# Performance work log

Measured on AMD Instinct MI355X. Metric: run time of the kernel, lower is better.

Reference implementation:

```python
import jax, jax.numpy as jnp
import numpy as np

DIM_IN = 1024
DIM_OUT = 1024


def setup_inputs() -> dict:
    key = jax.random.key(0)
    k1, k2, k3, k4 = jax.random.split(key, 4)
    X = jax.random.normal(k1, (4, 2048, DIM_IN), dtype=jnp.float32)
    s = 1.0 / np.sqrt(DIM_IN)
    Wq = jax.random.normal(k2, (DIM_IN, DIM_OUT), dtype=jnp.float32) * s
    Wk = jax.random.normal(k3, (DIM_IN, DIM_OUT), dtype=jnp.float32) * s
    Wv = jax.random.normal(k4, (DIM_IN, DIM_OUT), dtype=jnp.float32) * s
    return {"X": X, "Wq": Wq, "Wk": Wk, "Wv": Wv}


def reference(X, Wq, Wk, Wv):
    # X: [B, T, Din]; projections (qkv_bias=False)
    q = jnp.einsum('btd,de->bte', X, Wq)   # [B, T, Dout]
    k = jnp.einsum('btd,de->bte', X, Wk)
    v = jnp.einsum('btd,de->bte', X, Wv)
    T = X.shape[1]
    scores = jnp.einsum('bqe,bke->bqk', q, k)  # [B, T, T]
    causal = jnp.tril(jnp.ones((T, T), dtype=bool))  # mask upper triangle (future)
    scores = jnp.where(causal, scores, -jnp.inf)
    # scale=True: divide by sqrt(d); -inf stays -inf so order vs mask is irrelevant
    scores = scores / jnp.sqrt(jnp.asarray(k.shape[-1], dtype=scores.dtype))
    weights = jax.nn.softmax(scores, axis=-1)
    # dropout p=0.0 -> identity
    return jnp.einsum('bqk,bke->bqe', weights, v)
```

## Files before the change

kernel.cpp:

```cpp
#include <hip/hip_runtime.h>
#include <hip/hip_bf16.h>

typedef unsigned short u16;
typedef __bf16 bf16x8 __attribute__((ext_vector_type(8)));
typedef float f32x4 __attribute__((ext_vector_type(4)));
typedef unsigned short u16x8 __attribute__((ext_vector_type(8)));
typedef unsigned short u16x4 __attribute__((ext_vector_type(4)));

__device__ __forceinline__ float bf2f(u16 u) {
  unsigned int x = ((unsigned int)u) << 16;
  return __builtin_bit_cast(float, x);
}
__device__ __forceinline__ u16 f2bf(float f) {
  unsigned int x = __builtin_bit_cast(unsigned int, f);
  x = x + 0x7FFFu + ((x >> 16) & 1u);
  return (u16)(x >> 16);
}

__device__ __forceinline__ void gload_lds16(const u16* g, u16* l) {
  __builtin_amdgcn_global_load_lds(
      (const __attribute__((address_space(1))) unsigned int*)(unsigned long long)(uintptr_t)g,
      (__attribute__((address_space(3))) unsigned int*)(unsigned int)(uintptr_t)l,
      16, 0, 0);
}

__global__ __launch_bounds__(256) void prep_kernel(const float* __restrict__ X,
                                                   const float* __restrict__ Wq,
                                                   const float* __restrict__ Wk,
                                                   const float* __restrict__ Wv,
                                                   u16* __restrict__ Xb,
                                                   u16* __restrict__ Wqr,
                                                   u16* __restrict__ Wkr,
                                                   u16* __restrict__ WG) {
  const int id = blockIdx.x;
  const int tid = threadIdx.x;
  if (id < 5120) {
    const float* src;
    u16* dst;
    float scale = 1.0f;
    long i;
    if (id < 4096) {
      src = X; dst = Xb; i = ((long)id * 256 + tid) * 8;
    } else if (id < 4608) {
      src = Wq; dst = Wqr; scale = 1.0f / 32.0f;
      i = ((long)(id - 4096) * 256 + tid) * 8;
    } else {
      src = Wk; dst = Wkr;
      i = ((long)(id - 4608) * 256 + tid) * 8;
    }
    float4 a = *reinterpret_cast<const float4*>(src + i);
    float4 b = *reinterpret_cast<const float4*>(src + i + 4);
    u16x8 o;
    o[0] = f2bf(a.x * scale); o[1] = f2bf(a.y * scale);
    o[2] = f2bf(a.z * scale); o[3] = f2bf(a.w * scale);
    o[4] = f2bf(b.x * scale); o[5] = f2bf(b.y * scale);
    o[6] = f2bf(b.z * scale); o[7] = f2bf(b.w * scale);
    *reinterpret_cast<u16x8*>(dst + i) = o;
    return;
  }
  __shared__ u16 t[64][72];
  const int id2 = id - 5120;
  u16* out = WG + 1048576;
  const int c0 = (id2 & 15) * 64;
  const int r0 = (id2 >> 4) * 64;
#pragma unroll
  for (int i = 0; i < 4; ++i) {
    int slot = tid + 256 * i;
    int lr = slot >> 4;
    int lc4 = slot & 15;
    float4 v = *reinterpret_cast<const float4*>(Wv + (long)(r0 + lr) * 1024 + c0 + lc4 * 4);
    t[lr][lc4 * 4 + 0] = f2bf(v.x);
    t[lr][lc4 * 4 + 1] = f2bf(v.y);
    t[lr][lc4 * 4 + 2] = f2bf(v.z);
    t[lr][lc4 * 4 + 3] = f2bf(v.w);
  }
  __syncthreads();
#pragma unroll
  for (int i = 0; i < 2; ++i) {
    int slot = tid + 256 * i;
    int orow = slot >> 3;
    int oc = slot & 7;
    u16x8 o;
#pragma unroll
    for (int j = 0; j < 8; ++j) o[j] = t[oc * 8 + j][orow];
    *reinterpret_cast<u16x8*>(out + (long)(c0 + orow) * 1024 + r0 + oc * 8) = o;
  }
}

template <int MODE>
__global__ __launch_bounds__(256, 2) void gemm128(const u16* __restrict__ A,
                                                  const u16* __restrict__ B,
                                                  u16* __restrict__ C,
                                                  u16* __restrict__ Vt) {
  int bm, bn;
  if constexpr (MODE == 0) {
    bm = blockIdx.x >> 3;
    bn = blockIdx.x & 7;
  } else {
    const int id = blockIdx.x;
    const int xcd = id & 7, j = id >> 3;
    bn = (xcd & 1) * 8 + (j & 7);
    bm = ((xcd >> 1) << 4) + (j >> 3);
  }
  const int m0 = bm * 128, n0 = bn * 128;
  const int K = 1024;

  bool vblk = false;
  if constexpr (MODE == 1) vblk = (bn >> 3) == 1;

  __shared__ u16 ldsA[2][8192];
  __shared__ u16 ldsB[2][8192];

  const int tid = threadIdx.x;
  const int lane = tid & 63;
  const int wid = tid >> 6;
  const int wm = wid >> 1, wn = wid & 1;
  const int l16 = lane & 15, lh = lane >> 4;
  const int srow = lane >> 3;
  const int scol = ((lane & 7) ^ srow) * 8;
  const int rsw = l16 & 7;

  f32x4 acc[4][4];
#pragma unroll
  for (int mi = 0; mi < 4; ++mi)
#pragma unroll
    for (int ni = 0; ni < 4; ++ni) acc[mi][ni] = (f32x4)(0.0f);

  auto stage = [&](int d, int k0) {
#pragma unroll
    for (int s = 0; s < 4; ++s) {
      const int seg = wid * 4 + s;
      const int row = seg * 8 + srow;
      gload_lds16(A + (long)(m0 + row) * K + k0 + scol, &ldsA[d][seg * 512]);
      gload_lds16(B + (long)(n0 + row) * K + k0 + scol, &ldsB[d][seg * 512]);
    }
  };

  stage(0, 0);
  int cur = 0;
  for (int k0 = 0; k0 < K; k0 += 64) {
    __syncthreads();
    if (k0 + 64 < K) stage(cur ^ 1, k0 + 64);
#pragma unroll
    for (int kk = 0; kk < 2; ++kk) {
      bf16x8 af[4], bfr[4];
#pragma unroll
      for (int mi = 0; mi < 4; ++mi)
        af[mi] = *reinterpret_cast<const bf16x8*>(
            &ldsA[cur][(wm * 64 + mi * 16 + l16) * 64 + (((kk * 4 + lh) ^ rsw)) * 8]);
#pragma unroll
      for (int ni = 0; ni < 4; ++ni)
        bfr[ni] = *reinterpret_cast<const bf16x8*>(
            &ldsB[cur][(wn * 64 + ni * 16 + l16) * 64 + (((kk * 4 + lh) ^ rsw)) * 8]);
      if (!vblk) {
#pragma unroll
        for (int mi = 0; mi < 4; ++mi)
#pragma unroll
          for (int ni = 0; ni < 4; ++ni)
            acc[mi][ni] = __builtin_amdgcn_mfma_f32_16x16x32_bf16(bfr[ni], af[mi], acc[mi][ni], 0, 0, 0);
      } else {
#pragma unroll
        for (int mi = 0; mi < 4; ++mi)
#pragma unroll
          for (int ni = 0; ni < 4; ++ni)
            acc[mi][ni] = __builtin_amdgcn_mfma_f32_16x16x32_bf16(af[mi], bfr[ni], acc[mi][ni], 0, 0, 0);
      }
    }
    cur ^= 1;
  }

  if (!vblk) {
    const int col0 = (MODE == 0) ? n0 : (bn & 7) * 128;
    const long rown = (long)(m0 + wm * 64 + l16);
    const int coln = col0 + wn * 64 + lh * 4;
#pragma unroll
    for (int mi = 0; mi < 4; ++mi)
#pragma unroll
      for (int ni = 0; ni < 4; ++ni) {
        u16x4 o;
#pragma unroll
        for (int r = 0; r < 4; ++r) o[r] = f2bf(acc[mi][ni][r]);
        *reinterpret_cast<u16x4*>(&C[(rown + mi * 16) * 1024 + coln + ni * 16]) = o;
      }
  } else {
    const int b = m0 >> 11;
    const int t0 = (m0 & 2047) + wm * 64 + lh * 4;
    const int e0 = (bn & 7) * 128 + wn * 64 + l16;
#pragma unroll
    for (int mi = 0; mi < 4; ++mi)
#pragma unroll
      for (int ni = 0; ni < 4; ++ni) {
        u16x4 o;
#pragma unroll
        for (int r = 0; r < 4; ++r) o[r] = f2bf(acc[mi][ni][r]);
        *reinterpret_cast<u16x4*>(
            &Vt[(long)b * 2097152 + (long)(e0 + ni * 16) * 2048 + t0 + mi * 16]) = o;
      }
  }
}

__global__ __launch_bounds__(256, 3) void gemm_s(const u16* __restrict__ T1,
                                                 const u16* __restrict__ Xb,
                                                 u16* __restrict__ Sg,
                                                 float* __restrict__ Sums) {
  const int id = blockIdx.x;
  const int x = id & 7;
  const int q = id >> 3;
  const int bz = q / 34;
  int u = q - bz * 34;
  int qr, kc;
  const int n1 = 32 - 2 * x;
  if (u < n1) { kc = x;      qr = 2 * x + u; }
  else        { kc = 15 - x; qr = 30 - 2 * x + (u - n1); }
  const int m0 = qr * 64, n0 = kc * 128;
  const int K = 1024;

  const u16* A = T1 + (long)bz * 2097152;
  const u16* B = Xb + (long)bz * 2097152;

  __shared__ u16 ldsA[2][4096];
  __shared__ u16 ldsB[2][8192];

  const int tid = threadIdx.x;
  const int lane = tid & 63;
  const int wn = tid >> 6;
  const int l16 = lane & 15, lh = lane >> 4;
  const int strow = tid >> 3;
  const int scol = ((tid & 7) ^ (strow & 7)) * 8;
  const int rsw = l16 & 7;

  f32x4 acc[4][2];
#pragma unroll
  for (int mi = 0; mi < 4; ++mi)
#pragma unroll
    for (int ni = 0; ni < 2; ++ni) acc[mi][ni] = (f32x4)(0.0f);

  auto stage = [&](int d, int k0) {
#pragma unroll
    for (int l = 0; l < 2; ++l)
      gload_lds16(A + (long)(m0 + l * 32 + strow) * K + k0 + scol,
                  &ldsA[d][l * 2048 + tid * 8]);
#pragma unroll
    for (int l = 0; l < 4; ++l)
      gload_lds16(B + (long)(n0 + l * 32 + strow) * K + k0 + scol,
                  &ldsB[d][l * 2048 + tid * 8]);
  };

  stage(0, 0);
  int cur = 0;
  for (int k0 = 0; k0 < K; k0 += 64) {
    __syncthreads();
    if (k0 + 64 < K) stage(cur ^ 1, k0 + 64);
#pragma unroll
    for (int kk = 0; kk < 2; ++kk) {
      bf16x8 af[4], bfr[2];
#pragma unroll
      for (int mi = 0; mi < 4; ++mi)
        af[mi] = *reinterpret_cast<const bf16x8*>(
            &ldsA[cur][(mi * 16 + l16) * 64 + (((kk * 4 + lh) ^ rsw)) * 8]);
#pragma unroll
      for (int ni = 0; ni < 2; ++ni)
        bfr[ni] = *reinterpret_cast<const bf16x8*>(
            &ldsB[cur][(wn * 32 + ni * 16 + l16) * 64 + (((kk * 4 + lh) ^ rsw)) * 8]);
#pragma unroll
      for (int mi = 0; mi < 4; ++mi)
#pragma unroll
        for (int ni = 0; ni < 2; ++ni)
          acc[mi][ni] = __builtin_amdgcn_mfma_f32_16x16x32_bf16(bfr[ni], af[mi], acc[mi][ni], 0, 0, 0);
    }
    cur ^= 1;
  }

  u16* C = Sg + (long)bz * 4194304;
  float* sums = Sums + (long)bz * 2048;
  const int coln = n0 + wn * 32 + lh * 4;
#pragma unroll
  for (int mi = 0; mi < 4; ++mi) {
    const int gr = m0 + mi * 16 + l16;
    float rs = 0.0f;
#pragma unroll
    for (int ni = 0; ni < 2; ++ni) {
      u16x4 o;
#pragma unroll
      for (int r = 0; r < 4; ++r) {
        const int gc = coln + ni * 16 + r;
        const float e = (gc <= gr) ? __expf(acc[mi][ni][r]) : 0.0f;
        const u16 ub = f2bf(e);
        o[r] = ub;
        rs += bf2f(ub);
      }
      *reinterpret_cast<u16x4*>(&C[(long)gr * 2048 + coln + ni * 16]) = o;
    }
    rs += __shfl_xor(rs, 16);
    rs += __shfl_xor(rs, 32);
    if (lh == 0) atomicAdd(&sums[gr], rs);
  }
}

__global__ __launch_bounds__(512, 2) void gemm_pv(const u16* __restrict__ Ag,
                                                  const u16* __restrict__ Bg,
                                                  float* __restrict__ Cg,
                                                  const float* __restrict__ Sums) {
  const int id = blockIdx.x;
  const int x = id & 7;
  const int q = id >> 3;
  const int f = (q ^ (q >> 5)) & 1;
  const int i5 = ((q >> 1) & 15) | (((q >> 5) & 1) << 4);
  const int bmb = i5 & 7;
  const int bz = (i5 >> 3) & 3;
  const int bm = f ? (15 - bmb) : bmb;
  const int bn = x;
  const int K = 2048;

  const u16* A = Ag + (long)bz * 4194304;
  const u16* B = Bg + (long)bz * 2097152;
  const int m0 = bm * 128, n0 = bn * 128;
  const int kEnd = m0 + 128;

  __shared__ u16 ldsA[2][8192];
  __shared__ u16 ldsB[2][8192];

  const int tid = threadIdx.x;
  const int lane = tid & 63;
  const int wid = tid >> 6;
  const int wm = wid >> 2, wn = wid & 3;
  const int l16 = lane & 15, lh = lane >> 4;
  const int strow = tid >> 3;
  const int scol = ((tid & 7) ^ (strow & 7)) * 8;
  const int rsw = l16 & 7;

  f32x4 acc[4][2];
#pragma unroll
  for (int mi = 0; mi < 4; ++mi)
#pragma unroll
    for (int ni = 0; ni < 2; ++ni) acc[mi][ni] = (f32x4)(0.0f);

  auto stage = [&](int d, int k0) {
#pragma unroll
    for (int l = 0; l < 2; ++l) {
      const int row = l * 64 + strow;
      gload_lds16(A + (long)(m0 + row) * K + k0 + scol, &ldsA[d][l * 4096 + tid * 8]);
      gload_lds16(B + (long)(n0 + row) * K + k0 + scol, &ldsB[d][l * 4096 + tid * 8]);
    }
  };

  stage(0, 0);
  int cur = 0;
  for (int k0 = 0; k0 < kEnd; k0 += 64) {
    __syncthreads();
    if (k0 + 64 < kEnd) stage(cur ^ 1, k0 + 64);
#pragma unroll
    for (int kk = 0; kk < 2; ++kk) {
      bf16x8 af[4], bfr[2];
#pragma unroll
      for (int mi = 0; mi < 4; ++mi)
        af[mi] = *reinterpret_cast<const bf16x8*>(
            &ldsA[cur][(wm * 64 + mi * 16 + l16) * 64 + (((kk * 4 + lh) ^ rsw)) * 8]);
#pragma unroll
      for (int ni = 0; ni < 2; ++ni)
        bfr[ni] = *reinterpret_cast<const bf16x8*>(
            &ldsB[cur][(wn * 32 + ni * 16 + l16) * 64 + (((kk * 4 + lh) ^ rsw)) * 8]);
#pragma unroll
      for (int mi = 0; mi < 4; ++mi)
#pragma unroll
        for (int ni = 0; ni < 2; ++ni)
          acc[mi][ni] = __builtin_amdgcn_mfma_f32_16x16x32_bf16(bfr[ni], af[mi], acc[mi][ni], 0, 0, 0);
    }
    cur ^= 1;
  }

  float* C = Cg + (long)bz * 2097152;
  const float* sums = Sums + (long)bz * 2048;
  const long rown = (long)(m0 + wm * 64 + l16);
  const int coln = n0 + wn * 32 + lh * 4;
#pragma unroll
  for (int mi = 0; mi < 4; ++mi) {
    const float inv = 1.0f / sums[(int)rown + mi * 16];
#pragma unroll
    for (int ni = 0; ni < 2; ++ni) {
      f32x4 v = acc[mi][ni] * inv;
      *reinterpret_cast<f32x4*>(&C[(rown + mi * 16) * 1024 + coln + ni * 16]) = v;
    }
  }
}

extern "C" void kernel_launch(void* const* d_in, const int* in_sizes, int n_in,
                              void* d_out, int out_size, void* d_ws, size_t ws_size,
                              hipStream_t stream) {
  const float* X  = (const float*)d_in[0];
  const float* Wq = (const float*)d_in[1];
  const float* Wk = (const float*)d_in[2];
  const float* Wv = (const float*)d_in[3];

  u16* Xb  = (u16*)d_ws;
  u16* Wqr = Xb + 8388608;
  u16* Wkr = Wqr + 1048576;
  u16* WG  = Wkr + 1048576;
  u16* T1  = WG + 2097152;
  u16* Vt  = T1 + 8388608;
  u16* S   = Vt + 8388608;
  float* sums = (float*)(S + 16777216);

  hipMemsetAsync(sums, 0, 4 * 2048 * sizeof(float), stream);

  prep_kernel<<<5376, 256, 0, stream>>>(X, Wq, Wk, Wv, Xb, Wqr, Wkr, WG);

  gemm128<0><<<64, 256, 0, stream>>>(Wkr, Wqr, WG, nullptr);

  gemm128<1><<<1024, 256, 0, stream>>>(Xb, WG, T1, Vt);

  gemm_s<<<1088, 256, 0, stream>>>(T1, Xb, S, sums);

  gemm_pv<<<512, 512, 0, stream>>>(S, Vt, (float*)d_out, sums);
}
```

Measured before the change: 134.8 us.

## Fuse weight bf16 conversion into G GEMM and retile T1/V projection GEMM

The Wk/Wq fp32-to-bf16 conversion moves into the Wk·Wq^T GEMM, which now loads fp32 directly, converts in registers and stores to LDS. This drops the separate Wqr/Wkr buffers and their conversion pass in the prep kernel. The X·[G|Wv] projection GEMM is retiled from 128x128 blocks of 256 threads to 64x256 blocks of 512 threads, giving more reuse of each X tile against the wide weight panel. The new G GEMM has no double buffering, so its global loads are not overlapped with compute. The retiled kernel also uses more LDS per block, which may affect occupancy.

```diff
diff --git a/kernel.cpp b/kernel.cpp
--- a/kernel.cpp
+++ b/kernel.cpp
@@ -25,42 +25,23 @@
 }
 
 __global__ __launch_bounds__(256) void prep_kernel(const float* __restrict__ X,
-                                                   const float* __restrict__ Wq,
-                                                   const float* __restrict__ Wk,
                                                    const float* __restrict__ Wv,
                                                    u16* __restrict__ Xb,
-                                                   u16* __restrict__ Wqr,
-                                                   u16* __restrict__ Wkr,
-                                                   u16* __restrict__ WG) {
+                                                   u16* __restrict__ Wvt) {
   const int id = blockIdx.x;
   const int tid = threadIdx.x;
-  if (id < 5120) {
-    const float* src;
-    u16* dst;
-    float scale = 1.0f;
-    long i;
-    if (id < 4096) {
-      src = X; dst = Xb; i = ((long)id * 256 + tid) * 8;
-    } else if (id < 4608) {
-      src = Wq; dst = Wqr; scale = 1.0f / 32.0f;
-      i = ((long)(id - 4096) * 256 + tid) * 8;
-    } else {
-      src = Wk; dst = Wkr;
-      i = ((long)(id - 4608) * 256 + tid) * 8;
-    }
-    float4 a = *reinterpret_cast<const float4*>(src + i);
-    float4 b = *reinterpret_cast<const float4*>(src + i + 4);
+  if (id < 4096) {
+    long i = ((long)id * 256 + tid) * 8;
+    float4 a = *reinterpret_cast<const float4*>(X + i);
+    float4 b = *reinterpret_cast<const float4*>(X + i + 4);
     u16x8 o;
-    o[0] = f2bf(a.x * scale); o[1] = f2bf(a.y * scale);
-    o[2] = f2bf(a.z * scale); o[3] = f2bf(a.w * scale);
-    o[4] = f2bf(b.x * scale); o[5] = f2bf(b.y * scale);
-    o[6] = f2bf(b.z * scale); o[7] = f2bf(b.w * scale);
-    *reinterpret_cast<u16x8*>(dst + i) = o;
+    o[0] = f2bf(a.x); o[1] = f2bf(a.y); o[2] = f2bf(a.z); o[3] = f2bf(a.w);
+    o[4] = f2bf(b.x); o[5] = f2bf(b.y); o[6] = f2bf(b.z); o[7] = f2bf(b.w);
+    *reinterpret_cast<u16x8*>(Xb + i) = o;
     return;
   }
   __shared__ u16 t[64][72];
-  const int id2 = id - 5120;
-  u16* out = WG + 1048576;
+  const int id2 = id - 4096;
   const int c0 = (id2 & 15) * 64;
   const int r0 = (id2 >> 4) * 64;
 #pragma unroll
@@ -83,57 +64,128 @@
     u16x8 o;
 #pragma unroll
     for (int j = 0; j < 8; ++j) o[j] = t[oc * 8 + j][orow];
-    *reinterpret_cast<u16x8*>(out + (long)(c0 + orow) * 1024 + r0 + oc * 8) = o;
-  }
-}
-
-template <int MODE>
-__global__ __launch_bounds__(256, 2) void gemm128(const u16* __restrict__ A,
-                                                  const u16* __restrict__ B,
-                                                  u16* __restrict__ C,
-                                                  u16* __restrict__ Vt) {
-  int bm, bn;
-  if constexpr (MODE == 0) {
-    bm = blockIdx.x >> 3;
-    bn = blockIdx.x & 7;
-  } else {
-    const int id = blockIdx.x;
-    const int xcd = id & 7, j = id >> 3;
-    bn = (xcd & 1) * 8 + (j & 7);
-    bm = ((xcd >> 1) << 4) + (j >> 3);
-  }
+    *reinterpret_cast<u16x8*>(Wvt + (long)(c0 + orow) * 1024 + r0 + oc * 8) = o;
+  }
+}
+
+__global__ __launch_bounds__(256, 2) void gemm_g(const float* __restrict__ Wk,
+                                                 const float* __restrict__ Wq,
+                                                 u16* __restrict__ Gt) {
+  const int bm = blockIdx.x >> 3;
+  const int bn = blockIdx.x & 7;
   const int m0 = bm * 128, n0 = bn * 128;
-  const int K = 1024;
-
-  bool vblk = false;
-  if constexpr (MODE == 1) vblk = (bn >> 3) == 1;
-
-  __shared__ u16 ldsA[2][8192];
-  __shared__ u16 ldsB[2][8192];
+
+  __shared__ u16 ldsA[8192];
+  __shared__ u16 ldsB[8192];
 
   const int tid = threadIdx.x;
   const int lane = tid & 63;
   const int wid = tid >> 6;
   const int wm = wid >> 1, wn = wid & 1;
   const int l16 = lane & 15, lh = lane >> 4;
-  const int srow = lane >> 3;
-  const int scol = ((lane & 7) ^ srow) * 8;
+  const int csl = tid & 7;
+  const int rbase = tid >> 3;
+
+  f32x4 acc[4][4];
+#pragma unroll
+  for (int mi = 0; mi < 4; ++mi)
+#pragma unroll
+    for (int ni = 0; ni < 4; ++ni) acc[mi][ni] = (f32x4)(0.0f);
+
+  for (int k0 = 0; k0 < 1024; k0 += 64) {
+    __syncthreads();
+#pragma unroll
+    for (int c = 0; c < 4; ++c) {
+      const int row = c * 32 + rbase;
+      const int sp = (csl ^ (row & 7)) * 8;
+      float4 a0 = *reinterpret_cast<const float4*>(Wk + (long)(m0 + row) * 1024 + k0 + csl * 8);
+      float4 a1 = *reinterpret_cast<const float4*>(Wk + (long)(m0 + row) * 1024 + k0 + csl * 8 + 4);
+      u16x8 oa;
+      oa[0] = f2bf(a0.x); oa[1] = f2bf(a0.y); oa[2] = f2bf(a0.z); oa[3] = f2bf(a0.w);
+      oa[4] = f2bf(a1.x); oa[5] = f2bf(a1.y); oa[6] = f2bf(a1.z); oa[7] = f2bf(a1.w);
+      *reinterpret_cast<u16x8*>(&ldsA[row * 64 + sp]) = oa;
+      float4 b0 = *reinterpret_cast<const float4*>(Wq + (long)(n0 + row) * 1024 + k0 + csl * 8);
+      float4 b1 = *reinterpret_cast<const float4*>(Wq + (long)(n0 + row) * 1024 + k0 + csl * 8 + 4);
+      u16x8 ob;
+      const float s = 1.0f / 32.0f;
+      ob[0] = f2bf(b0.x * s); ob[1] = f2bf(b0.y * s); ob[2] = f2bf(b0.z * s); ob[3] = f2bf(b0.w * s);
+      ob[4] = f2bf(b1.x * s); ob[5] = f2bf(b1.y * s); ob[6] = f2bf(b1.z * s); ob[7] = f2bf(b1.w * s);
+      *reinterpret_cast<u16x8*>(&ldsB[row * 64 + sp]) = ob;
+    }
+    __syncthreads();
+#pragma unroll
+    for (int kk = 0; kk < 2; ++kk) {
+      bf16x8 af[4], bfr[4];
+#pragma unroll
+      for (int mi = 0; mi < 4; ++mi) {
+        const int row = wm * 64 + mi * 16 + l16;
+        af[mi] = *reinterpret_cast<const bf16x8*>(
+            &ldsA[row * 64 + (((kk * 4 + lh) ^ (row & 7))) * 8]);
+      }
+#pragma unroll
+      for (int ni = 0; ni < 4; ++ni) {
+        const int row = wn * 64 + ni * 16 + l16;
+        bfr[ni] = *reinterpret_cast<const bf16x8*>(
+            &ldsB[row * 64 + (((kk * 4 + lh) ^ (row & 7))) * 8]);
+      }
+#pragma unroll
+      for (int mi = 0; mi < 4; ++mi)
+#pragma unroll
+        for (int ni = 0; ni < 4; ++ni)
+          acc[mi][ni] = __builtin_amdgcn_mfma_f32_16x16x32_bf16(bfr[ni], af[mi], acc[mi][ni], 0, 0, 0);
+    }
+  }
+
+  const long rown = (long)(m0 + wm * 64 + l16);
+  const int coln = n0 + wn * 64 + lh * 4;
+#pragma unroll
+  for (int mi = 0; mi < 4; ++mi)
+#pragma unroll
+    for (int ni = 0; ni < 4; ++ni) {
+      u16x4 o;
+#pragma unroll
+      for (int r = 0; r < 4; ++r) o[r] = f2bf(acc[mi][ni][r]);
+      *reinterpret_cast<u16x4*>(&Gt[(rown + mi * 16) * 1024 + coln + ni * 16]) = o;
+    }
+}
+
+__global__ __launch_bounds__(512, 4) void gemm_t1v(const u16* __restrict__ Xb,
+                                                   const u16* __restrict__ WG,
+                                                   u16* __restrict__ T1,
+                                                   u16* __restrict__ Vt) {
+  const int id = blockIdx.x;
+  const int xcd = id & 7, j = id >> 3;
+  const int bn = (xcd & 1) * 4 + (j & 3);
+  const int bm = ((xcd >> 1) << 5) + (j >> 2);
+  const int m0 = bm * 64, n0 = bn * 256;
+  const int K = 1024;
+
+  __shared__ u16 ldsA[2][4096];
+  __shared__ u16 ldsB[2][16384];
+
+  const int tid = threadIdx.x;
+  const int lane = tid & 63;
+  const int wid = tid >> 6;
+  const int wm = wid >> 2, wn = wid & 3;
+  const int l16 = lane & 15, lh = lane >> 4;
+  const int strow = tid >> 3;
+  const int scol = ((tid & 7) ^ (strow & 7)) * 8;
   const int rsw = l16 & 7;
 
-  f32x4 acc[4][4];
-#pragma unroll
-  for (int mi = 0; mi < 4; ++mi)
+  const bool vblk = (bn >= 4);
+
+  f32x4 acc[2][4];
+#pragma unroll
+  for (int mi = 0; mi < 2; ++mi)
 #pragma unroll
     for (int ni = 0; ni < 4; ++ni) acc[mi][ni] = (f32x4)(0.0f);
 
   auto stage = [&](int d, int k0) {
-#pragma unroll
-    for (int s = 0; s < 4; ++s) {
-      const int seg = wid * 4 + s;
-      const int row = seg * 8 + srow;
-      gload_lds16(A + (long)(m0 + row) * K + k0 + scol, &ldsA[d][seg * 512]);
-      gload_lds16(B + (long)(n0 + row) * K + k0 + scol, &ldsB[d][seg * 512]);
-    }
+    gload_lds16(Xb + (long)(m0 + strow) * K + k0 + scol, &ldsA[d][tid * 8]);
+#pragma unroll
+    for (int l = 0; l < 4; ++l)
+      gload_lds16(WG + (long)(n0 + l * 64 + strow) * K + k0 + scol,
+                  &ldsB[d][l * 4096 + tid * 8]);
   };
 
   stage(0, 0);
@@ -143,24 +195,28 @@
     if (k0 + 64 < K) stage(cur ^ 1, k0 + 64);
 #pragma unroll
     for (int kk = 0; kk < 2; ++kk) {
-      bf16x8 af[4], bfr[4];
-#pragma unroll
-      for (int mi = 0; mi < 4; ++mi)
+      bf16x8 af[2], bfr[4];
+#pragma unroll
+      for (int mi = 0; mi < 2; ++mi) {
+        const int row = wm * 32 + mi * 16 + l16;
         af[mi] = *reinterpret_cast<const bf16x8*>(
-            &ldsA[cur][(wm * 64 + mi * 16 + l16) * 64 + (((kk * 4 + lh) ^ rsw)) * 8]);
-#pragma unroll
-      for (int ni = 0; ni < 4; ++ni)
+            &ldsA[cur][row * 64 + (((kk * 4 + lh) ^ rsw)) * 8]);
+      }
+#pragma unroll
+      for (int ni = 0; ni < 4; ++ni) {
+        const int row = wn * 64 + ni * 16 + l16;
         bfr[ni] = *reinterpret_cast<const bf16x8*>(
-            &ldsB[cur][(wn * 64 + ni * 16 + l16) * 64 + (((kk * 4 + lh) ^ rsw)) * 8]);
+            &ldsB[cur][row * 64 + (((kk * 4 + lh) ^ rsw)) * 8]);
+      }
       if (!vblk) {
 #pragma unroll
-        for (int mi = 0; mi < 4; ++mi)
+        for (int mi = 0; mi < 2; ++mi)
 #pragma unroll
           for (int ni = 0; ni < 4; ++ni)
             acc[mi][ni] = __builtin_amdgcn_mfma_f32_16x16x32_bf16(bfr[ni], af[mi], acc[mi][ni], 0, 0, 0);
       } else {
 #pragma unroll
-        for (int mi = 0; mi < 4; ++mi)
+        for (int mi = 0; mi < 2; ++mi)
 #pragma unroll
           for (int ni = 0; ni < 4; ++ni)
             acc[mi][ni] = __builtin_amdgcn_mfma_f32_16x16x32_bf16(af[mi], bfr[ni], acc[mi][ni], 0, 0, 0);
@@ -170,24 +226,23 @@
   }
 
   if (!vblk) {
-    const int col0 = (MODE == 0) ? n0 : (bn & 7) * 128;
-    const long rown = (long)(m0 + wm * 64 + l16);
-    const int coln = col0 + wn * 64 + lh * 4;
-#pragma unroll
-    for (int mi = 0; mi < 4; ++mi)
+    const long rown = (long)(m0 + wm * 32 + l16);
+    const int coln = bn * 256 + wn * 64 + lh * 4;
+#pragma unroll
+    for (int mi = 0; mi < 2; ++mi)
 #pragma unroll
       for (int ni = 0; ni < 4; ++ni) {
         u16x4 o;
 #pragma unroll
         for (int r = 0; r < 4; ++r) o[r] = f2bf(acc[mi][ni][r]);
-        *reinterpret_cast<u16x4*>(&C[(rown + mi * 16) * 1024 + coln + ni * 16]) = o;
+        *reinterpret_cast<u16x4*>(&T1[(rown + mi * 16) * 1024 + coln + ni * 16]) = o;
       }
   } else {
     const int b = m0 >> 11;
-    const int t0 = (m0 & 2047) + wm * 64 + lh * 4;
-    const int e0 = (bn & 7) * 128 + wn * 64 + l16;
-#pragma unroll
-    for (int mi = 0; mi < 4; ++mi)
+    const int t0 = (m0 & 2047) + wm * 32 + lh * 4;
+    const int e0 = (bn - 4) * 256 + wn * 64 + l16;
+#pragma unroll
+    for (int mi = 0; mi < 2; ++mi)
 #pragma unroll
       for (int ni = 0; ni < 4; ++ni) {
         u16x4 o;
@@ -392,22 +447,19 @@
   const float* Wk = (const float*)d_in[2];
   const float* Wv = (const float*)d_in[3];
 
-  u16* Xb  = (u16*)d_ws;
-  u16* Wqr = Xb + 8388608;
-  u16* Wkr = Wqr + 1048576;
-  u16* WG  = Wkr + 1048576;
-  u16* T1  = WG + 2097152;
-  u16* Vt  = T1 + 8388608;
-  u16* S   = Vt + 8388608;
+  u16* Xb = (u16*)d_ws;
+  u16* WG = Xb + 8388608;
+  u16* T1 = WG + 2097152;
+  u16* Vt = T1 + 8388608;
+  u16* S  = Vt + 8388608;
   float* sums = (float*)(S + 16777216);
 
   hipMemsetAsync(sums, 0, 4 * 2048 * sizeof(float), stream);
 
-  prep_kernel<<<5376, 256, 0, stream>>>(X, Wq, Wk, Wv, Xb, Wqr, Wkr, WG);
-
-  gemm128<0><<<64, 256, 0, stream>>>(Wkr, Wqr, WG, nullptr);
-
-  gemm128<1><<<1024, 256, 0, stream>>>(Xb, WG, T1, Vt);
+  gemm_g<<<64, 256, 0, stream>>>(Wk, Wq, WG);
+  prep_kernel<<<4352, 256, 0, stream>>>(X, Wv, Xb, WG + 1048576);
+
+  gemm_t1v<<<1024, 512, 0, stream>>>(Xb, WG, T1, Vt);
 
   gemm_s<<<1088, 256, 0, stream>>>(T1, Xb, S, sums);
 
```

Result: slower. 177.1 us (+31.4%).
